# Kernel tuning notes

Hardware: AMD Instinct MI355X
Metric: run time of the kernel (lower is better)

Reference implementation:

```python
import jax, jax.numpy as jnp
import numpy as np

A = 200.0          # penalty increment
NUM_STRUCT = 4     # classes 0..3: abutment, girder, deck, parapet
# (i, j, mult): weight[i]+=mult*A and weight[j]+=mult*A when GT says center_z_i < center_z_j
# but prediction says center_z_i >= center_z_j (and both classes present in GT and Pr).
PAIRS = [(0, 1, 1.0), (1, 2, 1.0), (2, 3, 1.0), (0, 2, 2.0), (1, 3, 2.0), (0, 3, 3.0)]


def setup_inputs() -> dict:
    key = jax.random.key(0)
    k1, k2, k3, k4, k5 = jax.random.split(key, 5)
    B, N, C = 16, 65536, 5
    pred = jax.random.normal(k1, (B, N, C), dtype=jnp.float32)
    target = jax.random.randint(k2, (B, N), 0, C, dtype=jnp.int32)
    points = jax.random.normal(k3, (B, N, 9), dtype=jnp.float32)
    pred_previous = jax.random.normal(k4, (B * N, C), dtype=jnp.float32)
    target_previous = jax.random.randint(k5, (B * N,), 0, C, dtype=jnp.int64)
    return {"pred": pred, "target": target, "points": points,
            "pred_previous": pred_previous, "target_previous": target_previous}


def _batch_weights(pred, target, points):
    """Per-batch class weights [B, C] following the original branch logic."""
    B, N, C = pred.shape
    z = points[:, :, 2]                                    # [B, N]
    pred_label = jnp.argmax(pred, axis=-1)                 # [B, N]
    cls = jnp.arange(NUM_STRUCT)
    gt_oh = (target[..., None] == cls).astype(z.dtype)     # [B, N, 4]
    pr_oh = (pred_label[..., None] == cls).astype(z.dtype)
    gt_cnt = gt_oh.sum(axis=1)                             # [B, 4]
    pr_cnt = pr_oh.sum(axis=1)
    gt_mean = jnp.einsum('bn,bnc->bc', z, gt_oh) / jnp.maximum(gt_cnt, 1.0)
    pr_mean = jnp.einsum('bn,bnc->bc', z, pr_oh) / jnp.maximum(pr_cnt, 1.0)
    GT = gt_cnt > 0
    PR = pr_cnt > 0

    w = jnp.ones((B, C), dtype=z.dtype)
    # class predicted but absent in GT
    miss = jnp.logical_and(jnp.logical_not(GT), PR).astype(z.dtype)  # [B, 4]
    w = w.at[:, :NUM_STRUCT].add(A * miss)
    # vertical-order violations
    for i, j, m in PAIRS:
        cond = (GT[:, i] & PR[:, i] & GT[:, j] & PR[:, j]
                & (gt_mean[:, i] < gt_mean[:, j])
                & (pr_mean[:, i] >= pr_mean[:, j]))
        add = (m * A) * cond.astype(z.dtype)
        w = w.at[:, i].add(add).at[:, j].add(add)
    return w


def reference(pred, target, points, pred_previous, target_previous):
    B, N, C = pred.shape
    w = _batch_weights(pred, target, points)               # [B, C]
    # weighted cross-entropy over pred_previous, computed once via per-class sums
    logp = jax.nn.log_softmax(pred_previous, axis=-1)      # [M, C]
    nll = -jnp.take_along_axis(logp, target_previous[:, None], axis=1)[:, 0]  # [M]
    s = jax.ops.segment_sum(nll, target_previous, num_segments=C)             # [C]
    n = jax.ops.segment_sum(jnp.ones_like(nll), target_previous, num_segments=C)
    # torch mean-reduction weighted CE: sum_n w[t_n]*nll_n / sum_n w[t_n]
    loss_b = (w @ s) / (w @ n)                             # [B]
    return loss_b.sum()
```

## Files before the change

kernel.cpp:

```cpp
#include <hip/hip_runtime.h>
#include <math.h>

#define A_W 200.0f
#define B_BATCH 16
#define N_PTS 65536
#define C_CLS 5
#define BN (B_BATCH * N_PTS)

#define BPB 64
#define STAT_BLOCKS (B_BATCH * BPB)
#define NLL_BLOCKS 512
#define TPB 256


__device__ inline float wave_reduce_f(float v) {
#pragma unroll
    for (int off = 32; off > 0; off >>= 1)
        v += __shfl_down(v, off, 64);
    return v;
}

__global__ void init_kernel(float* __restrict__ ws,
                            const unsigned* __restrict__ tprev_u32) {
    int t = threadIdx.x;
    if (t < 272) ws[t] = 0.0f;
    if (t == 0) {
        int is32 = 0;
        for (int i = 0; i < 64; ++i)
            is32 |= (tprev_u32[2 * i + 1] != 0u) ? 1 : 0;
        ((int*)ws)[272] = is32;
    }
}

__global__ __launch_bounds__(TPB)
void main_kernel(const float* __restrict__ pred,
                 const int* __restrict__ target,
                 const float* __restrict__ points,
                 const float* __restrict__ prev,
                 const void* __restrict__ tprev,
                 float* __restrict__ ws) {
    __shared__ float sm[16];
    const int bid = blockIdx.x;
    const int tid = threadIdx.x;
    const int lane = tid & 63;

    if (bid < STAT_BLOCKS) {
        const int b = bid / BPB;
        const int chunk = bid % BPB;
        const int per = N_PTS / BPB;
        const int n0 = chunk * per;
        const float* __restrict__ predb = pred + (size_t)b * N_PTS * C_CLS;
        const int* __restrict__ tgtb = target + (size_t)b * N_PTS;
        const float* __restrict__ ptsb = points + (size_t)b * N_PTS * 9;

        float gc0 = 0, gc1 = 0, gc2 = 0, gc3 = 0;
        float pc0 = 0, pc1 = 0, pc2 = 0, pc3 = 0;
        float gz0 = 0, gz1 = 0, gz2 = 0, gz3 = 0;
        float pz0 = 0, pz1 = 0, pz2 = 0, pz3 = 0;

        for (int n = n0 + tid; n < n0 + per; n += TPB) {
            const float* p = predb + (size_t)n * C_CLS;
            float x0 = p[0], x1 = p[1], x2 = p[2], x3 = p[3], x4 = p[4];
            int am = 0;
            float bv = x0;
            if (x1 > bv) { bv = x1; am = 1; }
            if (x2 > bv) { bv = x2; am = 2; }
            if (x3 > bv) { bv = x3; am = 3; }
            if (x4 > bv) { bv = x4; am = 4; }
            float z = ptsb[(size_t)n * 9 + 2];
            int t = tgtb[n];
            if (t == 0) { gc0 += 1.f; gz0 += z; }
            else if (t == 1) { gc1 += 1.f; gz1 += z; }
            else if (t == 2) { gc2 += 1.f; gz2 += z; }
            else if (t == 3) { gc3 += 1.f; gz3 += z; }
            if (am == 0) { pc0 += 1.f; pz0 += z; }
            else if (am == 1) { pc1 += 1.f; pz1 += z; }
            else if (am == 2) { pc2 += 1.f; pz2 += z; }
            else if (am == 3) { pc3 += 1.f; pz3 += z; }
        }

        if (tid < 16) sm[tid] = 0.0f;
        __syncthreads();

        float vals[16] = {gc0, gc1, gc2, gc3, pc0, pc1, pc2, pc3,
                          gz0, gz1, gz2, gz3, pz0, pz1, pz2, pz3};
#pragma unroll
        for (int k = 0; k < 16; ++k) {
            float r = wave_reduce_f(vals[k]);
            if (lane == 0) atomicAdd(&sm[k], r);
        }
        __syncthreads();
        if (tid < 16) atomicAdd(&ws[b * 16 + tid], sm[tid]);
    } else {
        const int nb = bid - STAT_BLOCKS;
        const int per = BN / NLL_BLOCKS;
        const int k0 = nb * per;
        const int flag32 = ((const int*)ws)[272];
        const int* __restrict__ tp32 = (const int*)tprev;
        const long long* __restrict__ tp64 = (const long long*)tprev;

        float s0 = 0, s1 = 0, s2 = 0, s3 = 0, s4 = 0;
        float c0 = 0, c1 = 0, c2 = 0, c3 = 0, c4 = 0;

        for (int k = k0 + tid; k < k0 + per; k += TPB) {
            const float* x = prev + (size_t)k * C_CLS;
            float x0 = x[0], x1 = x[1], x2 = x[2], x3 = x[3], x4 = x[4];
            float m = fmaxf(fmaxf(fmaxf(x0, x1), fmaxf(x2, x3)), x4);
            float e = expf(x0 - m) + expf(x1 - m) + expf(x2 - m) +
                      expf(x3 - m) + expf(x4 - m);
            float lse = m + logf(e);
            int t = flag32 ? tp32[k] : (int)tp64[k];
            float xt = x0;
            xt = (t == 1) ? x1 : xt;
            xt = (t == 2) ? x2 : xt;
            xt = (t == 3) ? x3 : xt;
            xt = (t == 4) ? x4 : xt;
            float nll = lse - xt;
            if (t == 0) { s0 += nll; c0 += 1.f; }
            else if (t == 1) { s1 += nll; c1 += 1.f; }
            else if (t == 2) { s2 += nll; c2 += 1.f; }
            else if (t == 3) { s3 += nll; c3 += 1.f; }
            else { s4 += nll; c4 += 1.f; }
        }

        if (tid < 16) sm[tid] = 0.0f;
        __syncthreads();

        float vals[10] = {s0, s1, s2, s3, s4, c0, c1, c2, c3, c4};
#pragma unroll
        for (int k = 0; k < 10; ++k) {
            float r = wave_reduce_f(vals[k]);
            if (lane == 0) atomicAdd(&sm[k], r);
        }
        __syncthreads();
        if (tid < 10) atomicAdd(&ws[256 + tid], sm[tid]);
    }
}

__global__ void final_kernel(const float* __restrict__ ws,
                             float* __restrict__ out) {
    const int lane = threadIdx.x;
    float loss = 0.0f;
    if (lane < B_BATCH) {
        const float* st = ws + lane * 16;
        float gc[4], pc[4], gz[4], pz[4];
        bool GT[4], PR[4];
        float gm[4], pm[4];
        float w[5] = {1.f, 1.f, 1.f, 1.f, 1.f};
#pragma unroll
        for (int c = 0; c < 4; ++c) {
            gc[c] = st[c];
            pc[c] = st[4 + c];
            gz[c] = st[8 + c];
            pz[c] = st[12 + c];
            GT[c] = gc[c] > 0.0f;
            PR[c] = pc[c] > 0.0f;
            gm[c] = gz[c] / fmaxf(gc[c], 1.0f);
            pm[c] = pz[c] / fmaxf(pc[c], 1.0f);
            if (!GT[c] && PR[c]) w[c] += A_W;
        }
#define PAIR(i, j, mlt)                                                        \
        {                                                                      \
            bool cond = GT[i] && PR[i] && GT[j] && PR[j] &&                    \
                        (gm[i] < gm[j]) && (pm[i] >= pm[j]);                   \
            float add = (mlt) * A_W * (cond ? 1.0f : 0.0f);                    \
            w[i] += add;                                                       \
            w[j] += add;                                                       \
        }
        PAIR(0, 1, 1.0f)
        PAIR(1, 2, 1.0f)
        PAIR(2, 3, 1.0f)
        PAIR(0, 2, 2.0f)
        PAIR(1, 3, 2.0f)
        PAIR(0, 3, 3.0f)
#undef PAIR
        const float* s = ws + 256;
        const float* n = ws + 261;
        float num = 0.0f, den = 0.0f;
#pragma unroll
        for (int c = 0; c < C_CLS; ++c) {
            num += w[c] * s[c];
            den += w[c] * n[c];
        }
        loss = num / den;
    }
#pragma unroll
    for (int off = 8; off > 0; off >>= 1)
        loss += __shfl_down(loss, off, 64);
    if (lane == 0) out[0] = loss;
}

extern "C" void kernel_launch(void* const* d_in, const int* in_sizes, int n_in,
                              void* d_out, int out_size, void* d_ws, size_t ws_size,
                              hipStream_t stream) {
    const float* pred = (const float*)d_in[0];
    const int* target = (const int*)d_in[1];
    const float* points = (const float*)d_in[2];
    const float* prev = (const float*)d_in[3];
    const void* tprev = d_in[4];
    float* ws = (float*)d_ws;
    float* out = (float*)d_out;

    hipLaunchKernelGGL(init_kernel, dim3(1), dim3(TPB), 0, stream,
                       ws, (const unsigned*)tprev);
    hipLaunchKernelGGL(main_kernel, dim3(STAT_BLOCKS + NLL_BLOCKS), dim3(TPB),
                       0, stream, pred, target, points, prev, tprev, ws);
    hipLaunchKernelGGL(final_kernel, dim3(1), dim3(64), 0, stream, ws, out);
}
```

Before: 120.1 us.

## Vectorize loads, drop init kernel, write per-block partials instead of atomics

Each thread now handles four consecutive points using float4/int4 loads, so the 5-float rows and targets are fetched with wide coalesced loads instead of strided scalar loads. The init kernel is removed: the int32/int64 target-format check moves into each NLL block as a ballot, and blocks write partial sums to distinct workspace slots rather than atomically accumulating into zeroed memory. The final kernel grows to 1024 threads and reduces those partials itself. This saves one launch and the global atomics, at the cost of more workspace and a larger single-block final reduction.

```diff
diff --git a/kernel.cpp b/kernel.cpp
--- a/kernel.cpp
+++ b/kernel.cpp
@@ -7,10 +7,10 @@
 #define C_CLS 5
 #define BN (B_BATCH * N_PTS)
 
-#define BPB 64
-#define STAT_BLOCKS (B_BATCH * BPB)
-#define NLL_BLOCKS 512
+#define STAT_BLOCKS 1024
+#define NLL_BLOCKS 1024
 #define TPB 256
+#define NLL_BASE 16384
 
 
 __device__ inline float wave_reduce_f(float v) {
@@ -18,18 +18,6 @@
     for (int off = 32; off > 0; off >>= 1)
         v += __shfl_down(v, off, 64);
     return v;
-}
-
-__global__ void init_kernel(float* __restrict__ ws,
-                            const unsigned* __restrict__ tprev_u32) {
-    int t = threadIdx.x;
-    if (t < 272) ws[t] = 0.0f;
-    if (t == 0) {
-        int is32 = 0;
-        for (int i = 0; i < 64; ++i)
-            is32 |= (tprev_u32[2 * i + 1] != 0u) ? 1 : 0;
-        ((int*)ws)[272] = is32;
-    }
 }
 
 __global__ __launch_bounds__(TPB)
@@ -37,38 +25,59 @@
                  const int* __restrict__ target,
                  const float* __restrict__ points,
                  const float* __restrict__ prev,
-                 const void* __restrict__ tprev,
+                 const unsigned* __restrict__ tprev_u32,
                  float* __restrict__ ws) {
     __shared__ float sm[16];
+    __shared__ int sflag;
     const int bid = blockIdx.x;
     const int tid = threadIdx.x;
     const int lane = tid & 63;
+    const int wv = tid >> 6;
+
+    if (tid < 16) sm[tid] = 0.0f;
+
+    if (bid >= STAT_BLOCKS && wv == 0) {
+        unsigned w = tprev_u32[2 * lane + 1];
+        unsigned long long bal = __ballot(w != 0u);
+        if (tid == 0) sflag = (bal != 0ull) ? 1 : 0;
+    }
+    __syncthreads();
 
     if (bid < STAT_BLOCKS) {
-        const int b = bid / BPB;
-        const int chunk = bid % BPB;
-        const int per = N_PTS / BPB;
-        const int n0 = chunk * per;
-        const float* __restrict__ predb = pred + (size_t)b * N_PTS * C_CLS;
-        const int* __restrict__ tgtb = target + (size_t)b * N_PTS;
-        const float* __restrict__ ptsb = points + (size_t)b * N_PTS * 9;
+        const int b = bid >> 6;
+        const int chunk = bid & 63;
+        const size_t n0 = (size_t)b * N_PTS + (size_t)chunk * 1024 + (size_t)tid * 4;
+
+        const float4* __restrict__ p4 = (const float4*)(pred + n0 * 5);
+        float4 q0 = p4[0], q1 = p4[1], q2 = p4[2], q3 = p4[3], q4 = p4[4];
+        const int4 tg = *(const int4*)(target + n0);
+        const float* __restrict__ pb = points + n0 * 9;
+        float zv[4] = {pb[2], pb[11], pb[20], pb[29]};
+
+        float xs[4][5] = {
+            {q0.x, q0.y, q0.z, q0.w, q1.x},
+            {q1.y, q1.z, q1.w, q2.x, q2.y},
+            {q2.z, q2.w, q3.x, q3.y, q3.z},
+            {q3.w, q4.x, q4.y, q4.z, q4.w}};
+        int tgt[4] = {tg.x, tg.y, tg.z, tg.w};
 
         float gc0 = 0, gc1 = 0, gc2 = 0, gc3 = 0;
         float pc0 = 0, pc1 = 0, pc2 = 0, pc3 = 0;
         float gz0 = 0, gz1 = 0, gz2 = 0, gz3 = 0;
         float pz0 = 0, pz1 = 0, pz2 = 0, pz3 = 0;
 
-        for (int n = n0 + tid; n < n0 + per; n += TPB) {
-            const float* p = predb + (size_t)n * C_CLS;
-            float x0 = p[0], x1 = p[1], x2 = p[2], x3 = p[3], x4 = p[4];
+#pragma unroll
+        for (int j = 0; j < 4; ++j) {
+            float x0 = xs[j][0], x1 = xs[j][1], x2 = xs[j][2],
+                  x3 = xs[j][3], x4 = xs[j][4];
             int am = 0;
             float bv = x0;
             if (x1 > bv) { bv = x1; am = 1; }
             if (x2 > bv) { bv = x2; am = 2; }
             if (x3 > bv) { bv = x3; am = 3; }
             if (x4 > bv) { bv = x4; am = 4; }
-            float z = ptsb[(size_t)n * 9 + 2];
-            int t = tgtb[n];
+            float z = zv[j];
+            int t = tgt[j];
             if (t == 0) { gc0 += 1.f; gz0 += z; }
             else if (t == 1) { gc1 += 1.f; gz1 += z; }
             else if (t == 2) { gc2 += 1.f; gz2 += z; }
@@ -79,9 +88,6 @@
             else if (am == 3) { pc3 += 1.f; pz3 += z; }
         }
 
-        if (tid < 16) sm[tid] = 0.0f;
-        __syncthreads();
-
         float vals[16] = {gc0, gc1, gc2, gc3, pc0, pc1, pc2, pc3,
                           gz0, gz1, gz2, gz3, pz0, pz1, pz2, pz3};
 #pragma unroll
@@ -90,26 +96,43 @@
             if (lane == 0) atomicAdd(&sm[k], r);
         }
         __syncthreads();
-        if (tid < 16) atomicAdd(&ws[b * 16 + tid], sm[tid]);
+        if (tid < 16) ws[(size_t)bid * 16 + tid] = sm[tid];
     } else {
         const int nb = bid - STAT_BLOCKS;
-        const int per = BN / NLL_BLOCKS;
-        const int k0 = nb * per;
-        const int flag32 = ((const int*)ws)[272];
-        const int* __restrict__ tp32 = (const int*)tprev;
-        const long long* __restrict__ tp64 = (const long long*)tprev;
+        const size_t k0 = (size_t)nb * 1024 + (size_t)tid * 4;
+        const int is32 = sflag;
+
+        const float4* __restrict__ p4 = (const float4*)(prev + k0 * 5);
+        float4 q0 = p4[0], q1 = p4[1], q2 = p4[2], q3 = p4[3], q4 = p4[4];
+
+        int tgt[4];
+        if (is32) {
+            int4 tt = *(const int4*)((const int*)tprev_u32 + k0);
+            tgt[0] = tt.x; tgt[1] = tt.y; tgt[2] = tt.z; tgt[3] = tt.w;
+        } else {
+            int4 a = *(const int4*)((const int*)tprev_u32 + 2 * k0);
+            int4 c = *(const int4*)((const int*)tprev_u32 + 2 * k0 + 4);
+            tgt[0] = a.x; tgt[1] = a.z; tgt[2] = c.x; tgt[3] = c.z;
+        }
+
+        float xs[4][5] = {
+            {q0.x, q0.y, q0.z, q0.w, q1.x},
+            {q1.y, q1.z, q1.w, q2.x, q2.y},
+            {q2.z, q2.w, q3.x, q3.y, q3.z},
+            {q3.w, q4.x, q4.y, q4.z, q4.w}};
 
         float s0 = 0, s1 = 0, s2 = 0, s3 = 0, s4 = 0;
         float c0 = 0, c1 = 0, c2 = 0, c3 = 0, c4 = 0;
 
-        for (int k = k0 + tid; k < k0 + per; k += TPB) {
-            const float* x = prev + (size_t)k * C_CLS;
-            float x0 = x[0], x1 = x[1], x2 = x[2], x3 = x[3], x4 = x[4];
+#pragma unroll
+        for (int j = 0; j < 4; ++j) {
+            float x0 = xs[j][0], x1 = xs[j][1], x2 = xs[j][2],
+                  x3 = xs[j][3], x4 = xs[j][4];
             float m = fmaxf(fmaxf(fmaxf(x0, x1), fmaxf(x2, x3)), x4);
             float e = expf(x0 - m) + expf(x1 - m) + expf(x2 - m) +
                       expf(x3 - m) + expf(x4 - m);
             float lse = m + logf(e);
-            int t = flag32 ? tp32[k] : (int)tp64[k];
+            int t = tgt[j];
             float xt = x0;
             xt = (t == 1) ? x1 : xt;
             xt = (t == 2) ? x2 : xt;
@@ -123,9 +146,6 @@
             else { s4 += nll; c4 += 1.f; }
         }
 
-        if (tid < 16) sm[tid] = 0.0f;
-        __syncthreads();
-
         float vals[10] = {s0, s1, s2, s3, s4, c0, c1, c2, c3, c4};
 #pragma unroll
         for (int k = 0; k < 10; ++k) {
@@ -133,30 +153,51 @@
             if (lane == 0) atomicAdd(&sm[k], r);
         }
         __syncthreads();
-        if (tid < 10) atomicAdd(&ws[256 + tid], sm[tid]);
-    }
-}
-
-__global__ void final_kernel(const float* __restrict__ ws,
-                             float* __restrict__ out) {
-    const int lane = threadIdx.x;
+        if (tid < 10) ws[NLL_BASE + (size_t)tid * 1024 + nb] = sm[tid];
+    }
+}
+
+__global__ __launch_bounds__(1024)
+void final_kernel(const float* __restrict__ ws, float* __restrict__ out) {
+    __shared__ float stat[256];
+    __shared__ float sn[10];
+    const int t = threadIdx.x;
+    const int lane = t & 63;
+    const int wv = t >> 6;
+
+    if (t < 256) {
+        const int b = t >> 4, v = t & 15;
+        const float* p = ws + (size_t)(b * 64) * 16 + v;
+        float s = 0.0f;
+#pragma unroll 8
+        for (int i = 0; i < 64; ++i) s += p[(size_t)i * 16];
+        stat[t] = s;
+    }
+    if (wv >= 4 && wv < 14) {
+        const int v = wv - 4;
+        const float* p = ws + NLL_BASE + (size_t)v * 1024;
+        float s = 0.0f;
+#pragma unroll
+        for (int k = 0; k < 16; ++k) s += p[lane + 64 * k];
+        s = wave_reduce_f(s);
+        if (lane == 0) sn[v] = s;
+    }
+    __syncthreads();
+
     float loss = 0.0f;
-    if (lane < B_BATCH) {
-        const float* st = ws + lane * 16;
-        float gc[4], pc[4], gz[4], pz[4];
+    if (t < B_BATCH) {
+        const float* st = stat + t * 16;
+        float gc[4], pc[4], gm[4], pm[4];
         bool GT[4], PR[4];
-        float gm[4], pm[4];
         float w[5] = {1.f, 1.f, 1.f, 1.f, 1.f};
 #pragma unroll
         for (int c = 0; c < 4; ++c) {
             gc[c] = st[c];
             pc[c] = st[4 + c];
-            gz[c] = st[8 + c];
-            pz[c] = st[12 + c];
             GT[c] = gc[c] > 0.0f;
             PR[c] = pc[c] > 0.0f;
-            gm[c] = gz[c] / fmaxf(gc[c], 1.0f);
-            pm[c] = pz[c] / fmaxf(pc[c], 1.0f);
+            gm[c] = st[8 + c] / fmaxf(gc[c], 1.0f);
+            pm[c] = st[12 + c] / fmaxf(pc[c], 1.0f);
             if (!GT[c] && PR[c]) w[c] += A_W;
         }
 #define PAIR(i, j, mlt)                                                        \
@@ -174,20 +215,20 @@
         PAIR(1, 3, 2.0f)
         PAIR(0, 3, 3.0f)
 #undef PAIR
-        const float* s = ws + 256;
-        const float* n = ws + 261;
         float num = 0.0f, den = 0.0f;
 #pragma unroll
         for (int c = 0; c < C_CLS; ++c) {
-            num += w[c] * s[c];
-            den += w[c] * n[c];
+            num += w[c] * sn[c];
+            den += w[c] * sn[5 + c];
         }
         loss = num / den;
     }
-#pragma unroll
-    for (int off = 8; off > 0; off >>= 1)
-        loss += __shfl_down(loss, off, 64);
-    if (lane == 0) out[0] = loss;
+    if (wv == 0) {
+#pragma unroll
+        for (int off = 8; off > 0; off >>= 1)
+            loss += __shfl_down(loss, off, 64);
+        if (t == 0) out[0] = loss;
+    }
 }
 
 extern "C" void kernel_launch(void* const* d_in, const int* in_sizes, int n_in,
@@ -197,13 +238,11 @@
     const int* target = (const int*)d_in[1];
     const float* points = (const float*)d_in[2];
     const float* prev = (const float*)d_in[3];
-    const void* tprev = d_in[4];
+    const unsigned* tprev = (const unsigned*)d_in[4];
     float* ws = (float*)d_ws;
     float* out = (float*)d_out;
 
-    hipLaunchKernelGGL(init_kernel, dim3(1), dim3(TPB), 0, stream,
-                       ws, (const unsigned*)tprev);
     hipLaunchKernelGGL(main_kernel, dim3(STAT_BLOCKS + NLL_BLOCKS), dim3(TPB),
                        0, stream, pred, target, points, prev, tprev, ws);
-    hipLaunchKernelGGL(final_kernel, dim3(1), dim3(64), 0, stream, ws, out);
-}
+    hipLaunchKernelGGL(final_kernel, dim3(1), dim3(1024), 0, stream, ws, out);
+}
```

After: 116.4 us. 1.03x faster.
